# Optimization experiments

Hardware: AMD Instinct MI355X
Metric: run time of the kernel (lower is better)

## Reference

```python
import jax, jax.numpy as jnp
import numpy as np

B, S, D, H, E, K = 2, 1024, 1024, 512, 16, 4  # batch, seq, hidden, expert inter, n_experts, top_k
HS = 2 * H  # shared expert inter dim = num_shared_experts * moe_inter_dim


def silu(z):
    return z * jax.nn.sigmoid(z)


def setup_inputs() -> dict:
    key = jax.random.key(0)
    ks = jax.random.split(key, 8)
    sc = lambda fan_in: 1.0 / np.sqrt(fan_in)
    x = jax.random.normal(ks[0], (B, S, D), jnp.float32)
    gate_w = jax.random.normal(ks[1], (E, D), jnp.float32) * sc(D)
    ws_in = jax.random.normal(ks[2], (D, HS), jnp.float32) * sc(D)
    vs_in = jax.random.normal(ks[3], (D, HS), jnp.float32) * sc(D)
    ws_out = jax.random.normal(ks[4], (HS, D), jnp.float32) * sc(HS)
    e_win = jax.random.normal(ks[5], (E, D, H), jnp.float32) * sc(D)
    e_vin = jax.random.normal(ks[6], (E, D, H), jnp.float32) * sc(D)
    e_wout = jax.random.normal(ks[7], (E, H, D), jnp.float32) * sc(H)
    return {"x": x, "gate_w": gate_w, "ws_in": ws_in, "vs_in": vs_in,
            "ws_out": ws_out, "e_win": e_win, "e_vin": e_vin, "e_wout": e_wout}


def reference(x, gate_w, ws_in, vs_in, ws_out, e_win, e_vin, e_wout):
    b, s, d = x.shape
    T = b * s
    xf = x.reshape(T, d)

    # --- Gate (eval path: biases buffer is zero / unused) ---
    g = jax.nn.sigmoid(xf @ gate_w.T)                      # [T, E]
    topv, topi = jax.lax.top_k(g, K)                        # [T, K]
    wn = topv / jnp.sum(topv, axis=-1, keepdims=True)       # normalized top-k weights
    # sparse combine matrix [T, E]: zero for unrouted experts -> exact same math
    # as the original per-expert masked gather/scatter loop
    combine = jnp.zeros_like(g).at[jnp.arange(T)[:, None], topi].add(wn)

    # --- Routed experts (SwiGLU), batched over experts ---
    hin = jnp.einsum('td,edh->eth', xf, e_win)              # [E, T, H]
    vin = jnp.einsum('td,edh->eth', xf, e_vin)              # [E, T, H]
    h = silu(hin) * vin * combine.T[:, :, None]             # weight before down-proj
    routed = jnp.einsum('eth,ehd->td', h, e_wout)           # [T, D]

    # --- Shared expert (SwiGLU with inter = num_shared * moe_inter) ---
    shared = (silu(xf @ ws_in) * (xf @ vs_in)) @ ws_out     # [T, D]

    return (shared + routed).reshape(b, s, d)
```

## Files before the change

kernel.cpp:

```cpp
#include <hip/hip_runtime.h>
#include <hip/hip_bf16.h>
#include <math.h>

typedef __attribute__((ext_vector_type(4))) float f32x4;
typedef __attribute__((ext_vector_type(8))) short s16x8;
typedef __hip_bfloat16 bf16;

constexpr int TOK = 2048;
constexpr int DIM = 1024;
constexpr int HID = 512;
constexpr int NE  = 16;
constexpr int NK  = 4;
constexpr int NHS = 1024;
constexpr int NPAIR = TOK * NK;

constexpr int UP_GRID = 128 + 4 * 80;
constexpr int DN_GRID = 64 + 4 * 80;

#define MFMA(a, b, c) __builtin_amdgcn_mfma_f32_16x16x32_bf16(a, b, c, 0, 0, 0)

#define GLOAD_LDS(gp, lp)                                                        \
  __builtin_amdgcn_global_load_lds(                                              \
      (const __attribute__((address_space(1))) unsigned int*)(gp),               \
      (__attribute__((address_space(3))) unsigned int*)(lp), 16, 0, 0)

template <int CH>
static __device__ __forceinline__ void stage_p(const bf16* const* rp, int k0,
                                               bf16* lds, int tid) {
  int wid = tid >> 6;
#pragma unroll
  for (int i = 0; i < CH; ++i) {
    int c = i * 512 + tid;
    int row = c >> 3;
    int slot = c & 7;
    int j = slot ^ (row & 7);
    const bf16* g = rp[i] + k0 + j * 8;
    bf16* l = lds + (size_t)(i * 512 + wid * 64) * 8;
    GLOAD_LDS(g, l);
  }
}

static __device__ __forceinline__ s16x8 frag(const bf16* lds, int row, int kc) {
  return *(const s16x8*)(lds + row * 64 + ((kc ^ (row & 7)) << 3));
}

struct bf16x4 { bf16 a, b, c, d; };


static __device__ __forceinline__ void tr_tile(const float* __restrict__ src,
                                               bf16* __restrict__ dst, int R, int C,
                                               int bx, int by, float t[32][33], int tid) {
  int tx = tid & 31, ty = tid >> 5;
  int c0 = bx * 32, r0 = by * 32;
#pragma unroll
  for (int i = 0; i < 32; i += 8) t[ty + i][tx] = src[(size_t)(r0 + ty + i) * C + c0 + tx];
  __syncthreads();
#pragma unroll
  for (int i = 0; i < 32; i += 8)
    dst[(size_t)(c0 + ty + i) * R + r0 + tx] = __float2bfloat16(t[tx][ty + i]);
}

__global__ __launch_bounds__(256) void prep1(const float* __restrict__ ws_in,
                                             const float* __restrict__ vs_in,
                                             const float* __restrict__ e_win,
                                             const float* __restrict__ e_vin,
                                             bf16* __restrict__ wsinT, bf16* __restrict__ vsinT,
                                             bf16* __restrict__ ewinT, bf16* __restrict__ evinT) {
  __shared__ float t[32][33];
  int bid = blockIdx.x, tid = threadIdx.x;
  if (bid < 1024) {
    tr_tile(ws_in, wsinT, DIM, NHS, bid & 31, bid >> 5, t, tid);
  } else if (bid < 2048) {
    int b = bid - 1024;
    tr_tile(vs_in, vsinT, DIM, NHS, b & 31, b >> 5, t, tid);
  } else if (bid < 10240) {
    int b = bid - 2048, e = b >> 9; b &= 511;
    tr_tile(e_win + (size_t)e * DIM * HID, ewinT + (size_t)e * DIM * HID,
            DIM, HID, b & 15, b >> 4, t, tid);
  } else {
    int b = bid - 10240, e = b >> 9; b &= 511;
    tr_tile(e_vin + (size_t)e * DIM * HID, evinT + (size_t)e * DIM * HID,
            DIM, HID, b & 15, b >> 4, t, tid);
  }
}

__global__ __launch_bounds__(256) void prep2(const float* __restrict__ ws_out,
                                             const float* __restrict__ e_wout,
                                             bf16* __restrict__ wsoutT,
                                             bf16* __restrict__ ewoutT) {
  __shared__ float t[32][33];
  int bid = blockIdx.x, tid = threadIdx.x;
  if (bid < 1024) {
    tr_tile(ws_out, wsoutT, NHS, DIM, bid & 31, bid >> 5, t, tid);
  } else {
    int b = bid - 1024, e = b >> 9; b &= 511;
    tr_tile(e_wout + (size_t)e * HID * DIM, ewoutT + (size_t)e * HID * DIM,
            HID, DIM, b & 31, b >> 5, t, tid);
  }
}


__global__ __launch_bounds__(256) void gate_scores(const float* __restrict__ x,
                                                   const float* __restrict__ gw,
                                                   bf16* __restrict__ xb,
                                                   float* __restrict__ scores) {
  int lane = threadIdx.x & 63, wid = threadIdx.x >> 6;
  int t = blockIdx.x * 4 + wid;
  const float* xr = x + (size_t)t * DIM + lane * 16;
  float4 x4[4];
#pragma unroll
  for (int q = 0; q < 4; ++q) x4[q] = *(const float4*)(xr + q * 4);
  {
    bf16* xo = xb + (size_t)t * DIM + lane * 16;
#pragma unroll
    for (int q = 0; q < 4; ++q) {
      bf16x4 o{__float2bfloat16(x4[q].x), __float2bfloat16(x4[q].y),
               __float2bfloat16(x4[q].z), __float2bfloat16(x4[q].w)};
      *reinterpret_cast<bf16x4*>(xo + q * 4) = o;
    }
  }
  float s[NE];
#pragma unroll
  for (int e = 0; e < NE; ++e) {
    const float* wr_ = gw + (size_t)e * DIM + lane * 16;
    float a = 0.f;
#pragma unroll
    for (int q = 0; q < 4; ++q) {
      float4 w4 = *(const float4*)(wr_ + q * 4);
      a += x4[q].x * w4.x + x4[q].y * w4.y + x4[q].z * w4.z + x4[q].w * w4.w;
    }
    s[e] = a;
  }
#pragma unroll
  for (int e = 0; e < NE; ++e)
#pragma unroll
    for (int off = 32; off; off >>= 1) s[e] += __shfl_xor(s[e], off);
  if (lane == 0) {
#pragma unroll
    for (int e = 0; e < NE; ++e) scores[(size_t)t * NE + e] = s[e];
  }
}

__global__ __launch_bounds__(256) void topk_hist(const float* __restrict__ scores,
                                                 int* __restrict__ topi,
                                                 float* __restrict__ topw,
                                                 int* __restrict__ counts) {
  __shared__ int h[NE];
  int tid = threadIdx.x;
  int t = blockIdx.x * 256 + tid;
  if (tid < NE) h[tid] = 0;
  __syncthreads();
  float g[NE];
  const float* sr = scores + (size_t)t * NE;
#pragma unroll
  for (int q = 0; q < 4; ++q) {
    float4 v = *(const float4*)(sr + q * 4);
    g[q * 4 + 0] = 1.f / (1.f + expf(-v.x));
    g[q * 4 + 1] = 1.f / (1.f + expf(-v.y));
    g[q * 4 + 2] = 1.f / (1.f + expf(-v.z));
    g[q * 4 + 3] = 1.f / (1.f + expf(-v.w));
  }
  unsigned used = 0;
  int bi[NK]; float bv[NK];
  float sum = 0.f;
#pragma unroll
  for (int j = 0; j < NK; ++j) {
    int best = 0; float v = -1e30f;
#pragma unroll
    for (int e = 0; e < NE; ++e)
      if (!((used >> e) & 1u) && g[e] > v) { v = g[e]; best = e; }
    used |= 1u << best; bi[j] = best; bv[j] = v; sum += v;
  }
  float inv = 1.f / sum;
#pragma unroll
  for (int j = 0; j < NK; ++j) {
    topi[t * NK + j] = bi[j];
    topw[t * NK + j] = bv[j] * inv;
    atomicAdd(&h[bi[j]], 1);
  }
  __syncthreads();
  if (tid < NE) atomicAdd(&counts[tid], h[tid]);
}

__global__ __launch_bounds__(64) void route_small(const int* __restrict__ counts,
                                                  int* __restrict__ offs,
                                                  int* __restrict__ segs,
                                                  int* __restrict__ nseg,
                                                  int* __restrict__ cursor) {
  if (threadIdx.x != 0) return;
  int o = 0;
#pragma unroll
  for (int e = 0; e < NE; ++e) { offs[e] = o; cursor[e * 32] = 0; o += counts[e]; }
  int s = 0;
  for (int e = 0; e < NE; ++e)
    for (int m = 0; m < counts[e]; m += 128) segs[s++] = (e << 16) | m;
  nseg[0] = s;
}

__global__ __launch_bounds__(256) void scatter_pairs(const int* __restrict__ topi,
                                                     const float* __restrict__ topw,
                                                     const int* __restrict__ offs,
                                                     int* __restrict__ cursor,
                                                     int* __restrict__ tok_list,
                                                     float* __restrict__ w_list) {
  int p = blockIdx.x * 256 + threadIdx.x;
  if (p >= NPAIR) return;
  int e = topi[p];
  int rank = atomicAdd(&cursor[e * 32], 1);
  int slot = offs[e] + rank;
  tok_list[slot] = p >> 2;
  w_list[slot] = topw[p];
}


__global__ __launch_bounds__(512, 4) void up_all(
    const bf16* __restrict__ xb, const bf16* __restrict__ wsinT,
    const bf16* __restrict__ vsinT, const bf16* __restrict__ ewinT,
    const bf16* __restrict__ evinT, const int* __restrict__ tok_list,
    const float* __restrict__ w_list, const int* __restrict__ counts,
    const int* __restrict__ offs, const int* __restrict__ segs,
    const int* __restrict__ nseg, bf16* __restrict__ hsb,
    bf16* __restrict__ hre) {
  int bid = blockIdx.x;
  int j = (bid & 7) * (UP_GRID / 8) + (bid >> 3);
  int nj = 128 + 4 * nseg[0];
  if (j >= nj) return;
  int tid = threadIdx.x, lane = tid & 63, wid = tid >> 6;
  int wr = wid >> 2, wc = wid & 3;

  bool is_shared = (j < 128);
  int m0, n0, cnt = TOK, off_e = 0;
  const bf16 *w1, *w2;
  if (is_shared) {
    m0 = (j >> 3) * 128; n0 = j & 7;
    w1 = wsinT; w2 = vsinT;
  } else {
    int r = j - 128;
    int sv = segs[r >> 2]; n0 = r & 3;
    int e = sv >> 16; m0 = sv & 0xffff;
    cnt = counts[e]; off_e = offs[e];
    w1 = ewinT + (size_t)e * HID * DIM;
    w2 = evinT + (size_t)e * HID * DIM;
  }

  const bf16* ap[2]; const bf16* bp[4];
#pragma unroll
  for (int i = 0; i < 2; ++i) {
    int row = (i * 512 + tid) >> 3;
    int gr = is_shared ? (m0 + row) : tok_list[off_e + min(m0 + row, cnt - 1)];
    ap[i] = xb + (size_t)gr * DIM;
  }
#pragma unroll
  for (int i = 0; i < 4; ++i) {
    int r = (i * 512 + tid) >> 3;
    int ridx = n0 * 128 + (r >> 5) * 16 + (r & 15);
    bp[i] = ((r & 16) ? w2 : w1) + (size_t)ridx * DIM;
  }

  __shared__ alignas(16) bf16 As[128 * 64], Bs[256 * 64];
  f32x4 acc[4][4];
  f32x4 z4 = {0.f, 0.f, 0.f, 0.f};
#pragma unroll
  for (int m = 0; m < 4; ++m)
#pragma unroll
    for (int q = 0; q < 4; ++q) acc[m][q] = z4;

  for (int k0 = 0; k0 < DIM; k0 += 64) {
    __syncthreads();
    stage_p<2>(ap, k0, As, tid);
    stage_p<4>(bp, k0, Bs, tid);
    __syncthreads();
#pragma unroll
    for (int ks = 0; ks < 2; ++ks) {
      int r16 = lane & 15, kc = (ks << 2) + (lane >> 4);
      s16x8 a[4];
#pragma unroll
      for (int m = 0; m < 4; ++m) a[m] = frag(As, wr * 64 + m * 16 + r16, kc);
#pragma unroll
      for (int q = 0; q < 4; ++q) {
        s16x8 b = frag(Bs, wc * 64 + q * 16 + r16, kc);
#pragma unroll
        for (int m = 0; m < 4; ++m) acc[m][q] = MFMA(a[m], b, acc[m][q]);
      }
    }
  }
#pragma unroll
  for (int m = 0; m < 4; ++m)
#pragma unroll
    for (int q = 0; q < 4; q += 2) {
      int c = n0 * 128 + (wc * 2 + (q >> 1)) * 16 + (lane & 15);
#pragma unroll
      for (int i = 0; i < 4; ++i) {
        int r = wr * 64 + m * 16 + (lane >> 4) * 4 + i;
        float z = acc[m][q][i], v = acc[m][q + 1][i];
        float h = z / (1.f + __expf(-z)) * v;
        if (is_shared) {
          hsb[(size_t)(m0 + r) * NHS + c] = __float2bfloat16(h);
        } else {
          int gr = m0 + r;
          if (gr < cnt)
            hre[(size_t)(off_e + gr) * HID + c] =
                __float2bfloat16(h * w_list[off_e + gr]);
        }
      }
    }
}


__global__ __launch_bounds__(512, 4) void down_all(
    const bf16* __restrict__ hsb, const bf16* __restrict__ wsoutT,
    const bf16* __restrict__ hre, const bf16* __restrict__ ewoutT,
    const int* __restrict__ tok_list, const int* __restrict__ counts,
    const int* __restrict__ offs, const int* __restrict__ segs,
    const int* __restrict__ nseg, float* __restrict__ out) {
  int bid = blockIdx.x;
  int j = (bid & 7) * (DN_GRID / 8) + (bid >> 3);
  int nj = 64 + 4 * nseg[0];
  if (j >= nj) return;
  int tid = threadIdx.x, lane = tid & 63, wid = tid >> 6;
  int wr = wid >> 2, wc = wid & 3;

  bool is_shared = (j < 64);
  int m0, n0, cnt = TOK, off_e = 0, K, ldA, ldB;
  const bf16 *Abase, *Bbase;
  if (is_shared) {
    m0 = (j >> 2) * 128; n0 = j & 3;
    Abase = hsb; ldA = NHS; K = NHS;
    Bbase = wsoutT; ldB = NHS;
  } else {
    int r = j - 64;
    int sv = segs[r >> 2]; n0 = r & 3;
    int e = sv >> 16; m0 = sv & 0xffff;
    cnt = counts[e]; off_e = offs[e];
    Abase = hre + (size_t)off_e * HID; ldA = HID; K = HID;
    Bbase = ewoutT + (size_t)e * DIM * HID; ldB = HID;
  }

  const bf16* ap[2]; const bf16* bp[4];
#pragma unroll
  for (int i = 0; i < 2; ++i) {
    int row = (i * 512 + tid) >> 3;
    int gr = is_shared ? (m0 + row) : min(m0 + row, cnt - 1);
    ap[i] = Abase + (size_t)gr * ldA;
  }
#pragma unroll
  for (int i = 0; i < 4; ++i) {
    int r = (i * 512 + tid) >> 3;
    bp[i] = Bbase + (size_t)(n0 * 256 + r) * ldB;
  }

  __shared__ alignas(16) bf16 As[128 * 64], Bs[256 * 64];
  f32x4 acc[4][4];
  f32x4 z4 = {0.f, 0.f, 0.f, 0.f};
#pragma unroll
  for (int m = 0; m < 4; ++m)
#pragma unroll
    for (int q = 0; q < 4; ++q) acc[m][q] = z4;

  int NT = K / 64;
  for (int kt = 0; kt < NT; ++kt) {
    int k0 = kt * 64;
    __syncthreads();
    stage_p<2>(ap, k0, As, tid);
    stage_p<4>(bp, k0, Bs, tid);
    __syncthreads();
#pragma unroll
    for (int ks = 0; ks < 2; ++ks) {
      int r16 = lane & 15, kc = (ks << 2) + (lane >> 4);
      s16x8 a[4];
#pragma unroll
      for (int m = 0; m < 4; ++m) a[m] = frag(As, wr * 64 + m * 16 + r16, kc);
#pragma unroll
      for (int q = 0; q < 4; ++q) {
        s16x8 b = frag(Bs, wc * 64 + q * 16 + r16, kc);
#pragma unroll
        for (int m = 0; m < 4; ++m) acc[m][q] = MFMA(a[m], b, acc[m][q]);
      }
    }
  }
#pragma unroll
  for (int m = 0; m < 4; ++m)
#pragma unroll
    for (int q = 0; q < 4; ++q) {
      int c = n0 * 256 + wc * 64 + q * 16 + (lane & 15);
#pragma unroll
      for (int i = 0; i < 4; ++i) {
        int r = wr * 64 + m * 16 + (lane >> 4) * 4 + i;
        if (is_shared) {
          atomicAdd(&out[(size_t)(m0 + r) * DIM + c], acc[m][q][i]);
        } else {
          int gr = m0 + r;
          if (gr < cnt)
            atomicAdd(&out[(size_t)tok_list[off_e + gr] * DIM + c], acc[m][q][i]);
        }
      }
    }
}


extern "C" void kernel_launch(void* const* d_in, const int* in_sizes, int n_in,
                              void* d_out, int out_size, void* d_ws, size_t ws_size,
                              hipStream_t stream) {
  const float* x      = (const float*)d_in[0];
  const float* gw     = (const float*)d_in[1];
  const float* ws_in  = (const float*)d_in[2];
  const float* vs_in  = (const float*)d_in[3];
  const float* ws_out = (const float*)d_in[4];
  const float* e_win  = (const float*)d_in[5];
  const float* e_vin  = (const float*)d_in[6];
  const float* e_wout = (const float*)d_in[7];
  float* out = (float*)d_out;

  char* p = (char*)d_ws;
  bf16* xb     = (bf16*)p;  p += (size_t)TOK * DIM * 2;
  bf16* wsinT  = (bf16*)p;
  bf16* wsoutT = wsinT;
  p += (size_t)NHS * DIM * 2;
  bf16* vsinT  = (bf16*)p;  p += (size_t)NHS * DIM * 2;
  bf16* hsb    = (bf16*)p;  p += (size_t)TOK * NHS * 2;
  bf16* ewinT  = (bf16*)p;
  bf16* ewoutT = ewinT;
  p += (size_t)NE * DIM * HID * 2;
  bf16* evinT  = (bf16*)p;  p += (size_t)NE * DIM * HID * 2;
  bf16* hre    = (bf16*)p;  p += (size_t)(NPAIR + 128) * HID * 2;
  int*   topi     = (int*)p;    p += (size_t)NPAIR * 4;
  float* topw     = (float*)p;  p += (size_t)NPAIR * 4;
  int*   tok_list = (int*)p;    p += (size_t)NPAIR * 4;
  float* w_list   = (float*)p;  p += (size_t)NPAIR * 4;
  float* scores   = (float*)p;  p += (size_t)TOK * NE * 4;
  int*   counts   = (int*)p;    p += 64;
  int*   offs     = (int*)p;    p += 64;
  int*   cursor   = (int*)p;    p += NE * 32 * 4;
  int*   segs     = (int*)p;    p += 128 * 4;
  int*   nseg     = (int*)p;    p += 64;

  hipMemsetAsync(counts, 0, NE * sizeof(int), stream);
  gate_scores<<<TOK / 4, 256, 0, stream>>>(x, gw, xb, scores);
  topk_hist<<<TOK / 256, 256, 0, stream>>>(scores, topi, topw, counts);
  route_small<<<1, 64, 0, stream>>>(counts, offs, segs, nseg, cursor);
  scatter_pairs<<<NPAIR / 256, 256, 0, stream>>>(topi, topw, offs, cursor,
                                                 tok_list, w_list);

  prep1<<<18432, 256, 0, stream>>>(ws_in, vs_in, e_win, e_vin,
                                   wsinT, vsinT, ewinT, evinT);

  up_all<<<UP_GRID, 512, 0, stream>>>(xb, wsinT, vsinT, ewinT, evinT, tok_list,
                                      w_list, counts, offs, segs, nseg, hsb, hre);

  prep2<<<9216, 256, 0, stream>>>(ws_out, e_wout, wsoutT, ewoutT);

  hipMemsetAsync(out, 0, (size_t)TOK * DIM * 4, stream);
  down_all<<<DN_GRID, 512, 0, stream>>>(hsb, wsoutT, hre, ewoutT, tok_list,
                                        counts, offs, segs, nseg, out);
}
```

Measured before the change: 166.0 us.

## Replace atomic scatter in down-projection with per-pair buffer and gather reduction

The down-projection now writes the shared-expert result straight into the output with plain stores. Each routed pair's result goes to a bf16 per-pair buffer, which reuses the expert v-weight storage that is no longer needed at that point. A new finish_add kernel uses a pair-to-slot map recorded during scattering to gather each token's four routed rows and add them to the output. This removes the output memset and millions of fp32 global atomics. In exchange it adds an extra kernel launch, an extra round trip through a 16 MB intermediate buffer, and bf16 rounding of routed partial sums before accumulation.

Result: faster. 143.8 us (-13.4%).

```diff
diff --git a/kernel.cpp b/kernel.cpp
--- a/kernel.cpp
+++ b/kernel.cpp
@@ -42,6 +42,12 @@
 
 static __device__ __forceinline__ s16x8 frag(const bf16* lds, int row, int kc) {
   return *(const s16x8*)(lds + row * 64 + ((kc ^ (row & 7)) << 3));
+}
+
+static __device__ __forceinline__ float b2f(short u) {
+  union { unsigned int i; float f; } c;
+  c.i = ((unsigned int)(unsigned short)u) << 16;
+  return c.f;
 }
 
 struct bf16x4 { bf16 a, b, c, d; };
@@ -202,7 +208,8 @@
                                                      const int* __restrict__ offs,
                                                      int* __restrict__ cursor,
                                                      int* __restrict__ tok_list,
-                                                     float* __restrict__ w_list) {
+                                                     float* __restrict__ w_list,
+                                                     int* __restrict__ pair_slot) {
   int p = blockIdx.x * 256 + threadIdx.x;
   if (p >= NPAIR) return;
   int e = topi[p];
@@ -210,6 +217,7 @@
   int slot = offs[e] + rank;
   tok_list[slot] = p >> 2;
   w_list[slot] = topw[p];
+  pair_slot[p] = slot;
 }
 
 
@@ -312,7 +320,8 @@
     const bf16* __restrict__ hre, const bf16* __restrict__ ewoutT,
     const int* __restrict__ tok_list, const int* __restrict__ counts,
     const int* __restrict__ offs, const int* __restrict__ segs,
-    const int* __restrict__ nseg, float* __restrict__ out) {
+    const int* __restrict__ nseg, float* __restrict__ out,
+    bf16* __restrict__ hrd) {
   int bid = blockIdx.x;
   int j = (bid & 7) * (DN_GRID / 8) + (bid >> 3);
   int nj = 64 + 4 * nseg[0];
@@ -387,14 +396,37 @@
       for (int i = 0; i < 4; ++i) {
         int r = wr * 64 + m * 16 + (lane >> 4) * 4 + i;
         if (is_shared) {
-          atomicAdd(&out[(size_t)(m0 + r) * DIM + c], acc[m][q][i]);
+          out[(size_t)(m0 + r) * DIM + c] = acc[m][q][i];
         } else {
           int gr = m0 + r;
           if (gr < cnt)
-            atomicAdd(&out[(size_t)tok_list[off_e + gr] * DIM + c], acc[m][q][i]);
+            hrd[(size_t)(off_e + gr) * DIM + c] = __float2bfloat16(acc[m][q][i]);
         }
       }
     }
+}
+
+
+__global__ __launch_bounds__(256) void finish_add(const bf16* __restrict__ hrd,
+                                                  const int* __restrict__ pair_slot,
+                                                  float* __restrict__ out) {
+  int idx = blockIdx.x * 256 + threadIdx.x;
+  int t = idx >> 7;
+  int c0 = (idx & 127) * 8;
+  int4 s4 = *(const int4*)(pair_slot + t * 4);
+  float acc[8];
+  float* o = out + (size_t)t * DIM + c0;
+#pragma unroll
+  for (int k = 0; k < 8; ++k) acc[k] = o[k];
+  int sl[4] = {s4.x, s4.y, s4.z, s4.w};
+#pragma unroll
+  for (int j = 0; j < 4; ++j) {
+    s16x8 v = *(const s16x8*)(hrd + (size_t)sl[j] * DIM + c0);
+#pragma unroll
+    for (int k = 0; k < 8; ++k) acc[k] += b2f(v[k]);
+  }
+#pragma unroll
+  for (int k = 0; k < 8; ++k) o[k] = acc[k];
 }
 
 
@@ -421,25 +453,28 @@
   bf16* ewinT  = (bf16*)p;
   bf16* ewoutT = ewinT;
   p += (size_t)NE * DIM * HID * 2;
-  bf16* evinT  = (bf16*)p;  p += (size_t)NE * DIM * HID * 2;
+  bf16* evinT  = (bf16*)p;
+  bf16* hrd    = evinT;
+  p += (size_t)NE * DIM * HID * 2;
   bf16* hre    = (bf16*)p;  p += (size_t)(NPAIR + 128) * HID * 2;
-  int*   topi     = (int*)p;    p += (size_t)NPAIR * 4;
-  float* topw     = (float*)p;  p += (size_t)NPAIR * 4;
-  int*   tok_list = (int*)p;    p += (size_t)NPAIR * 4;
-  float* w_list   = (float*)p;  p += (size_t)NPAIR * 4;
-  float* scores   = (float*)p;  p += (size_t)TOK * NE * 4;
-  int*   counts   = (int*)p;    p += 64;
-  int*   offs     = (int*)p;    p += 64;
-  int*   cursor   = (int*)p;    p += NE * 32 * 4;
-  int*   segs     = (int*)p;    p += 128 * 4;
-  int*   nseg     = (int*)p;    p += 64;
+  int*   topi      = (int*)p;    p += (size_t)NPAIR * 4;
+  float* topw      = (float*)p;  p += (size_t)NPAIR * 4;
+  int*   tok_list  = (int*)p;    p += (size_t)NPAIR * 4;
+  float* w_list    = (float*)p;  p += (size_t)NPAIR * 4;
+  int*   pair_slot = (int*)p;    p += (size_t)NPAIR * 4;
+  float* scores    = (float*)p;  p += (size_t)TOK * NE * 4;
+  int*   counts    = (int*)p;    p += 64;
+  int*   offs      = (int*)p;    p += 64;
+  int*   cursor    = (int*)p;    p += NE * 32 * 4;
+  int*   segs      = (int*)p;    p += 128 * 4;
+  int*   nseg      = (int*)p;    p += 64;
 
   hipMemsetAsync(counts, 0, NE * sizeof(int), stream);
   gate_scores<<<TOK / 4, 256, 0, stream>>>(x, gw, xb, scores);
   topk_hist<<<TOK / 256, 256, 0, stream>>>(scores, topi, topw, counts);
   route_small<<<1, 64, 0, stream>>>(counts, offs, segs, nseg, cursor);
   scatter_pairs<<<NPAIR / 256, 256, 0, stream>>>(topi, topw, offs, cursor,
-                                                 tok_list, w_list);
+                                                 tok_list, w_list, pair_slot);
 
   prep1<<<18432, 256, 0, stream>>>(ws_in, vs_in, e_win, e_vin,
                                    wsinT, vsinT, ewinT, evinT);
@@ -449,7 +484,7 @@
 
   prep2<<<9216, 256, 0, stream>>>(ws_out, e_wout, wsoutT, ewoutT);
 
-  hipMemsetAsync(out, 0, (size_t)TOK * DIM * 4, stream);
   down_all<<<DN_GRID, 512, 0, stream>>>(hsb, wsoutT, hre, ewoutT, tok_list,
-                                        counts, offs, segs, nseg, out);
-}
+                                        counts, offs, segs, nseg, out, hrd);
+  finish_add<<<TOK * DIM / 8 / 256, 256, 0, stream>>>(hrd, pair_slot, out);
+}
```
